# Optimization experiments

Measured on AMD Instinct MI355X. Metric: run time of the kernel, lower is better.

## Reference

```python
import jax, jax.numpy as jnp
import numpy as np

B, D = 16384, 2048          # batch, input_dim
N_TOP, N_CLASS = 8, 16      # top labels, bottom labels per top (uniform, contiguous ids)

def setup_inputs() -> dict:
    key = jax.random.key(0)
    k1, k2, k3, k4, k5 = jax.random.split(key, 5)
    INIT = 0.2  # matches init_weight uniform(-0.2, 0.2)
    return {
        "features": jax.random.normal(k1, (B, D), dtype=jnp.float32),
        "top_W": jax.random.uniform(k2, (N_TOP, D), minval=-INIT, maxval=INIT, dtype=jnp.float32),
        "top_b": jax.random.uniform(k3, (N_TOP,), minval=-INIT, maxval=INIT, dtype=jnp.float32),
        "bottom_W": jax.random.uniform(k4, (N_TOP, D, N_CLASS), minval=-INIT, maxval=INIT, dtype=jnp.float32),
        "bottom_b": jax.random.uniform(k5, (N_TOP, N_CLASS), minval=-INIT, maxval=INIT, dtype=jnp.float32),
    }

def reference(features, top_W, top_b, bottom_W, bottom_b):
    # dropout p=0.0 -> identity
    # top gate: linear + sigmoid, (b, n_top)
    top_scores = jax.nn.sigmoid(features @ top_W.T + top_b)
    # all per-top-label expert linears as one batched GEMM: (b, n_top, n_class)
    bottom_logits = jnp.einsum('bd,tdc->btc', features, bottom_W) + bottom_b
    bottom_scores = jax.nn.softmax(bottom_logits, axis=-1)
    # scatter-combine: bottom ids of top i are contiguous [i*N_CLASS, (i+1)*N_CLASS),
    # so the column scatter is a reshape. (b, n_bottom_labels)
    final_scores = (top_scores[:, :, None] * bottom_scores).reshape(features.shape[0], N_TOP * N_CLASS)
    return final_scores
```

## Files before the change

### kernel.cpp

```cpp
#include <hip/hip_runtime.h>


#define D_DIM 2048
#define NTILE 9
#define M_ROWS 16

using f32x4 = float __attribute__((ext_vector_type(4)));
using half8 = _Float16 __attribute__((ext_vector_type(8)));
using fp16x2 = __fp16 __attribute__((ext_vector_type(2)));

__global__ void prep_weights(const float* __restrict__ topW,
                             const float* __restrict__ botW,
                             _Float16* __restrict__ S) {
    int idx = blockIdx.x * blockDim.x + threadIdx.x;
    if (idx >= 4 * 16 * NTILE * 64) return;
    int lane = idx & 63;
    int tmp  = idx >> 6;
    int nt   = tmp % NTILE;
    int wks  = tmp / NTILE;
    int n     = nt * 16 + (lane & 15);
    int kbase = wks * 32 + (lane >> 4) * 8;

    _Float16 v[8];
    #pragma unroll
    for (int j = 0; j < 8; j++) {
        int k = kbase + j;
        float x = 0.0f;
        if (n < 8) {
            x = topW[n * D_DIM + k];
        } else if (n < 136) {
            int t = (n - 8) >> 4, c = (n - 8) & 15;
            x = botW[(t * D_DIM + k) * 16 + c];
        }
        v[j] = (_Float16)x;
    }
    *(half8*)(S + (size_t)idx * 8) = *(half8*)v;
}

static __device__ __forceinline__ half8 pack_af(f32x4 a, f32x4 b) {
    fp16x2 p0 = __builtin_amdgcn_cvt_pkrtz(a[0], a[1]);
    fp16x2 p1 = __builtin_amdgcn_cvt_pkrtz(a[2], a[3]);
    fp16x2 p2 = __builtin_amdgcn_cvt_pkrtz(b[0], b[1]);
    fp16x2 p3 = __builtin_amdgcn_cvt_pkrtz(b[2], b[3]);
    half8 r;
    r[0] = (_Float16)p0[0]; r[1] = (_Float16)p0[1];
    r[2] = (_Float16)p1[0]; r[3] = (_Float16)p1[1];
    r[4] = (_Float16)p2[0]; r[5] = (_Float16)p2[1];
    r[6] = (_Float16)p3[0]; r[7] = (_Float16)p3[1];
    return r;
}

#define GL4(dst, voff, sbase, IMM)                                         \
    asm volatile("global_load_dwordx4 %0, %1, %2 offset:%3"                \
                 : "=v"(dst) : "v"(voff), "s"(sbase), "i"(IMM))

#define VWAIT(N) do {                                                      \
        asm volatile("s_waitcnt vmcnt(%0)" :: "i"(N) : "memory");          \
        __builtin_amdgcn_sched_barrier(0);                                 \
    } while (0)

__global__ __launch_bounds__(256, 4) void hc_fused(
        const float* __restrict__ feat, const _Float16* __restrict__ Bsw,
        const float* __restrict__ top_b, const float* __restrict__ bot_b,
        float* __restrict__ out) {
    __shared__ float red[4][M_ROWS][148];

    const int tid  = threadIdx.x;
    const int lane = tid & 63, wave = tid >> 6;
    const int quad = lane >> 4, low = lane & 15;
    const size_t row0 = (size_t)blockIdx.x * M_ROWS;

    const unsigned long long sA = (unsigned long long)feat;
    const unsigned long long sB = (unsigned long long)Bsw;
    const unsigned vAoff = (unsigned)(((row0 + low) * D_DIM + wave * 512 + quad * 8) * 4);
    const unsigned vBoff = (unsigned)(wave * 147456 + lane * 16);

    f32x4 acc[NTILE];
    #pragma unroll
    for (int i = 0; i < NTILE; i++) acc[i] = (f32x4)0.0f;

    f32x4 b0_, b1_, b2_, b3_, b4_, b5_, b6_, b7_, b8_;
    f32x4 aX0, aX1, aY0, aY1;

#define ISSUE_B(KS) do {                                                   \
        unsigned off_lo_ = vBoff + ((KS) * 9216 + 2048);                   \
        unsigned off_hi_ = vBoff + ((KS) * 9216 + 6144);                   \
        GL4(b0_, off_lo_, sB, -2048);                                      \
        GL4(b1_, off_lo_, sB, -1024);                                      \
        GL4(b2_, off_lo_, sB,     0);                                      \
        GL4(b3_, off_lo_, sB,  1024);                                      \
        GL4(b4_, off_hi_, sB, -2048);                                      \
        GL4(b5_, off_hi_, sB, -1024);                                      \
        GL4(b6_, off_hi_, sB,     0);                                      \
        GL4(b7_, off_hi_, sB,  1024);                                      \
        GL4(b8_, off_hi_, sB,  2048);                                      \
    } while (0)

#define COMP(AL0, AL1) do {                                                \
        const half8 af_ = pack_af(AL0, AL1);                               \
        acc[0] = __builtin_amdgcn_mfma_f32_16x16x32_f16(af_, __builtin_bit_cast(half8, b0_), acc[0], 0, 0, 0); \
        acc[1] = __builtin_amdgcn_mfma_f32_16x16x32_f16(af_, __builtin_bit_cast(half8, b1_), acc[1], 0, 0, 0); \
        acc[2] = __builtin_amdgcn_mfma_f32_16x16x32_f16(af_, __builtin_bit_cast(half8, b2_), acc[2], 0, 0, 0); \
        acc[3] = __builtin_amdgcn_mfma_f32_16x16x32_f16(af_, __builtin_bit_cast(half8, b3_), acc[3], 0, 0, 0); \
        acc[4] = __builtin_amdgcn_mfma_f32_16x16x32_f16(af_, __builtin_bit_cast(half8, b4_), acc[4], 0, 0, 0); \
        acc[5] = __builtin_amdgcn_mfma_f32_16x16x32_f16(af_, __builtin_bit_cast(half8, b5_), acc[5], 0, 0, 0); \
        acc[6] = __builtin_amdgcn_mfma_f32_16x16x32_f16(af_, __builtin_bit_cast(half8, b6_), acc[6], 0, 0, 0); \
        acc[7] = __builtin_amdgcn_mfma_f32_16x16x32_f16(af_, __builtin_bit_cast(half8, b7_), acc[7], 0, 0, 0); \
        acc[8] = __builtin_amdgcn_mfma_f32_16x16x32_f16(af_, __builtin_bit_cast(half8, b8_), acc[8], 0, 0, 0); \
        __builtin_amdgcn_sched_barrier(0);                                 \
    } while (0)

    ISSUE_B(0);
    GL4(aX0, vAoff, sA,   0);  GL4(aX1, vAoff, sA,  16);
    GL4(aY0, vAoff, sA, 128);  GL4(aY1, vAoff, sA, 144);

    VWAIT(2); COMP(aX0, aX1); ISSUE_B( 1); GL4(aX0, vAoff, sA,  256); GL4(aX1, vAoff, sA,  272);
    VWAIT(2); COMP(aY0, aY1); ISSUE_B( 2); GL4(aY0, vAoff, sA,  384); GL4(aY1, vAoff, sA,  400);
    VWAIT(2); COMP(aX0, aX1); ISSUE_B( 3); GL4(aX0, vAoff, sA,  512); GL4(aX1, vAoff, sA,  528);
    VWAIT(2); COMP(aY0, aY1); ISSUE_B( 4); GL4(aY0, vAoff, sA,  640); GL4(aY1, vAoff, sA,  656);
    VWAIT(2); COMP(aX0, aX1); ISSUE_B( 5); GL4(aX0, vAoff, sA,  768); GL4(aX1, vAoff, sA,  784);
    VWAIT(2); COMP(aY0, aY1); ISSUE_B( 6); GL4(aY0, vAoff, sA,  896); GL4(aY1, vAoff, sA,  912);
    VWAIT(2); COMP(aX0, aX1); ISSUE_B( 7); GL4(aX0, vAoff, sA, 1024); GL4(aX1, vAoff, sA, 1040);
    VWAIT(2); COMP(aY0, aY1); ISSUE_B( 8); GL4(aY0, vAoff, sA, 1152); GL4(aY1, vAoff, sA, 1168);
    VWAIT(2); COMP(aX0, aX1); ISSUE_B( 9); GL4(aX0, vAoff, sA, 1280); GL4(aX1, vAoff, sA, 1296);
    VWAIT(2); COMP(aY0, aY1); ISSUE_B(10); GL4(aY0, vAoff, sA, 1408); GL4(aY1, vAoff, sA, 1424);
    VWAIT(2); COMP(aX0, aX1); ISSUE_B(11); GL4(aX0, vAoff, sA, 1536); GL4(aX1, vAoff, sA, 1552);
    VWAIT(2); COMP(aY0, aY1); ISSUE_B(12); GL4(aY0, vAoff, sA, 1664); GL4(aY1, vAoff, sA, 1680);
    VWAIT(2); COMP(aX0, aX1); ISSUE_B(13); GL4(aX0, vAoff, sA, 1792); GL4(aX1, vAoff, sA, 1808);
    VWAIT(2); COMP(aY0, aY1); ISSUE_B(14); GL4(aY0, vAoff, sA, 1920); GL4(aY1, vAoff, sA, 1936);
    VWAIT(2); COMP(aX0, aX1); ISSUE_B(15);
    VWAIT(0); COMP(aY0, aY1);

#undef ISSUE_B
#undef COMP

    #pragma unroll
    for (int nt = 0; nt < NTILE; nt++) {
        #pragma unroll
        for (int r = 0; r < 4; r++) {
            red[wave][quad * 4 + r][nt * 16 + low] = acc[nt][r];
        }
    }
    __syncthreads();

    if (tid < 128) {
        const int row = tid >> 3;
        const int top = tid & 7;

        float zt = top_b[top];
        #pragma unroll
        for (int w = 0; w < 4; w++) zt += red[w][row][top];
        const float sig = 1.0f / (1.0f + __expf(-zt));

        float z[16];
        float zmax = -1e30f;
        #pragma unroll
        for (int c = 0; c < 16; c++) {
            float v = bot_b[top * 16 + c];
            #pragma unroll
            for (int w = 0; w < 4; w++) v += red[w][row][8 + top * 16 + c];
            z[c] = v;
            zmax = fmaxf(zmax, v);
        }
        float s = 0.0f;
        #pragma unroll
        for (int c = 0; c < 16; c++) { z[c] = __expf(z[c] - zmax); s += z[c]; }
        const float scale = sig / s;

        float* o = out + (row0 + row) * 128 + top * 16;
        #pragma unroll
        for (int c = 0; c < 16; c += 4) {
            f32x4 v = { z[c] * scale, z[c+1] * scale, z[c+2] * scale, z[c+3] * scale };
            *(f32x4*)(o + c) = v;
        }
    }
}

extern "C" void kernel_launch(void* const* d_in, const int* in_sizes, int n_in,
                              void* d_out, int out_size, void* d_ws, size_t ws_size,
                              hipStream_t stream) {
    const float* feat  = (const float*)d_in[0];
    const float* topW  = (const float*)d_in[1];
    const float* topB  = (const float*)d_in[2];
    const float* botW  = (const float*)d_in[3];
    const float* botB  = (const float*)d_in[4];
    float* out = (float*)d_out;
    _Float16* Bsw = (_Float16*)d_ws;

    prep_weights<<<(4 * 16 * NTILE * 64 + 255) / 256, 256, 0, stream>>>(topW, botW, Bsw);
    hc_fused<<<16384 / M_ROWS, 256, 0, stream>>>(feat, Bsw, topB, botB, out);
}
```

Baseline: 223.1 us.

## Share staged weight tiles in LDS across waves, each wave owning 16 rows

The GEMM is reorganized so each block handles 64 rows, with each wave computing 16 full rows over the whole K dimension, instead of splitting K across waves for 16 rows. Weight tiles are streamed into a triple-buffered LDS ring with global_load_lds and shared by all four waves. This cuts redundant global weight loads per output row and removes the cross-wave K reduction in the epilogue. In exchange it adds block barriers every K step, uses more LDS, and lowers the occupancy target from 4 to 2.

```diff
diff --git a/kernel.cpp b/kernel.cpp
--- a/kernel.cpp
+++ b/kernel.cpp
@@ -3,7 +3,9 @@
 
 #define D_DIM 2048
 #define NTILE 9
-#define M_ROWS 16
+#define M_ROWS 64
+#define STEP_HALFS 6144
+#define NSTEPS 64
 
 using f32x4 = float __attribute__((ext_vector_type(4)));
 using half8 = _Float16 __attribute__((ext_vector_type(8)));
@@ -13,13 +15,13 @@
                              const float* __restrict__ botW,
                              _Float16* __restrict__ S) {
     int idx = blockIdx.x * blockDim.x + threadIdx.x;
-    if (idx >= 4 * 16 * NTILE * 64) return;
+    if (idx >= NSTEPS * NTILE * 64) return;
     int lane = idx & 63;
     int tmp  = idx >> 6;
     int nt   = tmp % NTILE;
-    int wks  = tmp / NTILE;
+    int KS   = tmp / NTILE;
     int n     = nt * 16 + (lane & 15);
-    int kbase = wks * 32 + (lane >> 4) * 8;
+    int kbase = KS * 32 + (lane >> 4) * 8;
 
     _Float16 v[8];
     #pragma unroll
@@ -34,7 +36,7 @@
         }
         v[j] = (_Float16)x;
     }
-    *(half8*)(S + (size_t)idx * 8) = *(half8*)v;
+    *(half8*)(S + (size_t)KS * STEP_HALFS + (size_t)(nt * 64 + lane) * 8) = *(half8*)v;
 }
 
 static __device__ __forceinline__ half8 pack_af(f32x4 a, f32x4 b) {
@@ -59,80 +61,99 @@
         __builtin_amdgcn_sched_barrier(0);                                 \
     } while (0)
 
-__global__ __launch_bounds__(256, 4) void hc_fused(
+#define SB() __builtin_amdgcn_sched_barrier(0)
+#define BAR() do { __builtin_amdgcn_s_barrier();                           \
+                   __builtin_amdgcn_sched_barrier(0); } while (0)
+
+typedef __attribute__((address_space(1))) const void gv_t;
+typedef __attribute__((address_space(3))) void lv_t;
+
+__global__ __launch_bounds__(256, 2) void hc_fused(
         const float* __restrict__ feat, const _Float16* __restrict__ Bsw,
         const float* __restrict__ top_b, const float* __restrict__ bot_b,
         float* __restrict__ out) {
-    __shared__ float red[4][M_ROWS][148];
+    __shared__ _Float16 bufB[3][STEP_HALFS];
+    __shared__ float red[4][16][148];
 
     const int tid  = threadIdx.x;
     const int lane = tid & 63, wave = tid >> 6;
     const int quad = lane >> 4, low = lane & 15;
-    const size_t row0 = (size_t)blockIdx.x * M_ROWS;
+    const int rowg0 = blockIdx.x * M_ROWS + wave * 16;
 
     const unsigned long long sA = (unsigned long long)feat;
-    const unsigned long long sB = (unsigned long long)Bsw;
-    const unsigned vAoff = (unsigned)(((row0 + low) * D_DIM + wave * 512 + quad * 8) * 4);
-    const unsigned vBoff = (unsigned)(wave * 147456 + lane * 16);
+    const unsigned aBase = (unsigned)(((unsigned)(rowg0 + low) * D_DIM + quad * 8) * 4);
 
     f32x4 acc[NTILE];
     #pragma unroll
     for (int i = 0; i < NTILE; i++) acc[i] = (f32x4)0.0f;
 
-    f32x4 b0_, b1_, b2_, b3_, b4_, b5_, b6_, b7_, b8_;
     f32x4 aX0, aX1, aY0, aY1;
 
-#define ISSUE_B(KS) do {                                                   \
-        unsigned off_lo_ = vBoff + ((KS) * 9216 + 2048);                   \
-        unsigned off_hi_ = vBoff + ((KS) * 9216 + 6144);                   \
-        GL4(b0_, off_lo_, sB, -2048);                                      \
-        GL4(b1_, off_lo_, sB, -1024);                                      \
-        GL4(b2_, off_lo_, sB,     0);                                      \
-        GL4(b3_, off_lo_, sB,  1024);                                      \
-        GL4(b4_, off_hi_, sB, -2048);                                      \
-        GL4(b5_, off_hi_, sB, -1024);                                      \
-        GL4(b6_, off_hi_, sB,     0);                                      \
-        GL4(b7_, off_hi_, sB,  1024);                                      \
-        GL4(b8_, off_hi_, sB,  2048);                                      \
+#define STAGE(GSRC, SLOT) do {                                             \
+        const _Float16* g_ = (GSRC) + (size_t)tid * 8;                     \
+        _Pragma("unroll")                                                  \
+        for (int r_ = 0; r_ < 3; r_++) {                                   \
+            __builtin_amdgcn_global_load_lds(                              \
+                (gv_t*)(g_ + r_ * 2048),                                   \
+                (lv_t*)&bufB[SLOT][(unsigned)(r_ * 256 + wave * 64) * 8],  \
+                16, 0, 0);                                                 \
+        }                                                                  \
     } while (0)
 
-#define COMP(AL0, AL1) do {                                                \
+#define COMPUTE(SLOT, AL0, AL1) do {                                       \
+        const _Float16* Lp_ = &bufB[SLOT][(unsigned)lane * 8];             \
+        half8 f0_ = *(const half8*)(Lp_);                                  \
+        half8 f1_ = *(const half8*)(Lp_ +  512);                           \
+        half8 f2_ = *(const half8*)(Lp_ + 1024);                           \
+        half8 f3_ = *(const half8*)(Lp_ + 1536);                           \
+        half8 f4_ = *(const half8*)(Lp_ + 2048);                           \
+        half8 f5_ = *(const half8*)(Lp_ + 2560);                           \
+        half8 f6_ = *(const half8*)(Lp_ + 3072);                           \
+        half8 f7_ = *(const half8*)(Lp_ + 3584);                           \
+        half8 f8_ = *(const half8*)(Lp_ + 4096);                           \
         const half8 af_ = pack_af(AL0, AL1);                               \
-        acc[0] = __builtin_amdgcn_mfma_f32_16x16x32_f16(af_, __builtin_bit_cast(half8, b0_), acc[0], 0, 0, 0); \
-        acc[1] = __builtin_amdgcn_mfma_f32_16x16x32_f16(af_, __builtin_bit_cast(half8, b1_), acc[1], 0, 0, 0); \
-        acc[2] = __builtin_amdgcn_mfma_f32_16x16x32_f16(af_, __builtin_bit_cast(half8, b2_), acc[2], 0, 0, 0); \
-        acc[3] = __builtin_amdgcn_mfma_f32_16x16x32_f16(af_, __builtin_bit_cast(half8, b3_), acc[3], 0, 0, 0); \
-        acc[4] = __builtin_amdgcn_mfma_f32_16x16x32_f16(af_, __builtin_bit_cast(half8, b4_), acc[4], 0, 0, 0); \
-        acc[5] = __builtin_amdgcn_mfma_f32_16x16x32_f16(af_, __builtin_bit_cast(half8, b5_), acc[5], 0, 0, 0); \
-        acc[6] = __builtin_amdgcn_mfma_f32_16x16x32_f16(af_, __builtin_bit_cast(half8, b6_), acc[6], 0, 0, 0); \
-        acc[7] = __builtin_amdgcn_mfma_f32_16x16x32_f16(af_, __builtin_bit_cast(half8, b7_), acc[7], 0, 0, 0); \
-        acc[8] = __builtin_amdgcn_mfma_f32_16x16x32_f16(af_, __builtin_bit_cast(half8, b8_), acc[8], 0, 0, 0); \
-        __builtin_amdgcn_sched_barrier(0);                                 \
+        acc[0] = __builtin_amdgcn_mfma_f32_16x16x32_f16(af_, f0_, acc[0], 0, 0, 0); \
+        acc[1] = __builtin_amdgcn_mfma_f32_16x16x32_f16(af_, f1_, acc[1], 0, 0, 0); \
+        acc[2] = __builtin_amdgcn_mfma_f32_16x16x32_f16(af_, f2_, acc[2], 0, 0, 0); \
+        acc[3] = __builtin_amdgcn_mfma_f32_16x16x32_f16(af_, f3_, acc[3], 0, 0, 0); \
+        acc[4] = __builtin_amdgcn_mfma_f32_16x16x32_f16(af_, f4_, acc[4], 0, 0, 0); \
+        acc[5] = __builtin_amdgcn_mfma_f32_16x16x32_f16(af_, f5_, acc[5], 0, 0, 0); \
+        acc[6] = __builtin_amdgcn_mfma_f32_16x16x32_f16(af_, f6_, acc[6], 0, 0, 0); \
+        acc[7] = __builtin_amdgcn_mfma_f32_16x16x32_f16(af_, f7_, acc[7], 0, 0, 0); \
+        acc[8] = __builtin_amdgcn_mfma_f32_16x16x32_f16(af_, f8_, acc[8], 0, 0, 0); \
     } while (0)
 
-    ISSUE_B(0);
-    GL4(aX0, vAoff, sA,   0);  GL4(aX1, vAoff, sA,  16);
-    GL4(aY0, vAoff, sA, 128);  GL4(aY1, vAoff, sA, 144);
-
-    VWAIT(2); COMP(aX0, aX1); ISSUE_B( 1); GL4(aX0, vAoff, sA,  256); GL4(aX1, vAoff, sA,  272);
-    VWAIT(2); COMP(aY0, aY1); ISSUE_B( 2); GL4(aY0, vAoff, sA,  384); GL4(aY1, vAoff, sA,  400);
-    VWAIT(2); COMP(aX0, aX1); ISSUE_B( 3); GL4(aX0, vAoff, sA,  512); GL4(aX1, vAoff, sA,  528);
-    VWAIT(2); COMP(aY0, aY1); ISSUE_B( 4); GL4(aY0, vAoff, sA,  640); GL4(aY1, vAoff, sA,  656);
-    VWAIT(2); COMP(aX0, aX1); ISSUE_B( 5); GL4(aX0, vAoff, sA,  768); GL4(aX1, vAoff, sA,  784);
-    VWAIT(2); COMP(aY0, aY1); ISSUE_B( 6); GL4(aY0, vAoff, sA,  896); GL4(aY1, vAoff, sA,  912);
-    VWAIT(2); COMP(aX0, aX1); ISSUE_B( 7); GL4(aX0, vAoff, sA, 1024); GL4(aX1, vAoff, sA, 1040);
-    VWAIT(2); COMP(aY0, aY1); ISSUE_B( 8); GL4(aY0, vAoff, sA, 1152); GL4(aY1, vAoff, sA, 1168);
-    VWAIT(2); COMP(aX0, aX1); ISSUE_B( 9); GL4(aX0, vAoff, sA, 1280); GL4(aX1, vAoff, sA, 1296);
-    VWAIT(2); COMP(aY0, aY1); ISSUE_B(10); GL4(aY0, vAoff, sA, 1408); GL4(aY1, vAoff, sA, 1424);
-    VWAIT(2); COMP(aX0, aX1); ISSUE_B(11); GL4(aX0, vAoff, sA, 1536); GL4(aX1, vAoff, sA, 1552);
-    VWAIT(2); COMP(aY0, aY1); ISSUE_B(12); GL4(aY0, vAoff, sA, 1664); GL4(aY1, vAoff, sA, 1680);
-    VWAIT(2); COMP(aX0, aX1); ISSUE_B(13); GL4(aX0, vAoff, sA, 1792); GL4(aX1, vAoff, sA, 1808);
-    VWAIT(2); COMP(aY0, aY1); ISSUE_B(14); GL4(aY0, vAoff, sA, 1920); GL4(aY1, vAoff, sA, 1936);
-    VWAIT(2); COMP(aX0, aX1); ISSUE_B(15);
-    VWAIT(0); COMP(aY0, aY1);
-
-#undef ISSUE_B
-#undef COMP
+    STAGE(Bsw, 0); SB();
+    GL4(aX0, aBase, sA, 0);   GL4(aX1, aBase, sA, 16);  SB();
+    STAGE(Bsw + STEP_HALFS, 1); SB();
+    GL4(aY0, aBase, sA, 128); GL4(aY1, aBase, sA, 144); SB();
+
+    unsigned aoffX = aBase + 256;
+    unsigned aoffY = aBase + 384;
+    const _Float16* gS = Bsw + (size_t)2 * STEP_HALFS;
+    int se = 0, so = 1;
+
+    for (int i = 0; i < 31; ++i) {
+        VWAIT(5); BAR();
+        COMPUTE(se, aX0, aX1);
+        SB();
+        int we = se - 1; if (we < 0) we += 3;
+        STAGE(gS, we); gS += STEP_HALFS; SB();
+        GL4(aX0, aoffX, sA, 0); GL4(aX1, aoffX, sA, 16); aoffX += 256; SB();
+        se = we;
+        VWAIT(5); BAR();
+        COMPUTE(so, aY0, aY1);
+        SB();
+        int wo = so - 1; if (wo < 0) wo += 3;
+        STAGE(gS, wo); gS += STEP_HALFS; SB();
+        GL4(aY0, aoffY, sA, 0); GL4(aY1, aoffY, sA, 16); aoffY += 256; SB();
+        so = wo;
+    }
+    VWAIT(5); BAR(); COMPUTE(se, aX0, aX1);
+    VWAIT(0); BAR(); COMPUTE(so, aY0, aY1);
+
+#undef STAGE
+#undef COMPUTE
 
     #pragma unroll
     for (int nt = 0; nt < NTILE; nt++) {
@@ -143,35 +164,34 @@
     }
     __syncthreads();
 
-    if (tid < 128) {
-        const int row = tid >> 3;
-        const int top = tid & 7;
-
-        float zt = top_b[top];
+    {
+        const int row = lane & 15;
+        const int q2  = lane >> 4;
         #pragma unroll
-        for (int w = 0; w < 4; w++) zt += red[w][row][top];
-        const float sig = 1.0f / (1.0f + __expf(-zt));
-
-        float z[16];
-        float zmax = -1e30f;
-        #pragma unroll
-        for (int c = 0; c < 16; c++) {
-            float v = bot_b[top * 16 + c];
+        for (int tt = 0; tt < 2; tt++) {
+            const int t = q2 * 2 + tt;
+            float zt = red[wave][row][t] + top_b[t];
+            const float sig = 1.0f / (1.0f + __expf(-zt));
+
+            float z[16];
+            float zmax = -1e30f;
             #pragma unroll
-            for (int w = 0; w < 4; w++) v += red[w][row][8 + top * 16 + c];
-            z[c] = v;
-            zmax = fmaxf(zmax, v);
-        }
-        float s = 0.0f;
-        #pragma unroll
-        for (int c = 0; c < 16; c++) { z[c] = __expf(z[c] - zmax); s += z[c]; }
-        const float scale = sig / s;
-
-        float* o = out + (row0 + row) * 128 + top * 16;
-        #pragma unroll
-        for (int c = 0; c < 16; c += 4) {
-            f32x4 v = { z[c] * scale, z[c+1] * scale, z[c+2] * scale, z[c+3] * scale };
-            *(f32x4*)(o + c) = v;
+            for (int c = 0; c < 16; c++) {
+                float v = red[wave][row][8 + t * 16 + c] + bot_b[t * 16 + c];
+                z[c] = v;
+                zmax = fmaxf(zmax, v);
+            }
+            float s = 0.0f;
+            #pragma unroll
+            for (int c = 0; c < 16; c++) { z[c] = __expf(z[c] - zmax); s += z[c]; }
+            const float scale = sig / s;
+
+            float* o = out + (size_t)(rowg0 + row) * 128 + t * 16;
+            #pragma unroll
+            for (int c = 0; c < 16; c += 4) {
+                f32x4 v = { z[c] * scale, z[c+1] * scale, z[c+2] * scale, z[c+3] * scale };
+                *(f32x4*)(o + c) = v;
+            }
         }
     }
 }
@@ -187,6 +207,6 @@
     float* out = (float*)d_out;
     _Float16* Bsw = (_Float16*)d_ws;
 
-    prep_weights<<<(4 * 16 * NTILE * 64 + 255) / 256, 256, 0, stream>>>(topW, botW, Bsw);
+    prep_weights<<<(NSTEPS * NTILE * 64 + 255) / 256, 256, 0, stream>>>(topW, botW, Bsw);
     hc_fused<<<16384 / M_ROWS, 256, 0, stream>>>(feat, Bsw, topB, botB, out);
 }
```

Measured after the change: 223.1 us. Within noise of the previous version (+0.0%).
